# Kernel tuning notes

Measured on AMD Instinct MI355X. Metric: run time of the kernel, lower is better.

## Reference

```python
import jax, jax.numpy as jnp
import numpy as np

HIDDEN = 768
HEADS = 12
HEAD_DIM = HIDDEN // HEADS  # 64


def setup_inputs() -> dict:
    key = jax.random.key(0)
    ks = jax.random.split(key, 8)
    B, S = 2, 2048
    hidden_states = jax.random.normal(ks[0], (B, S, HIDDEN), dtype=jnp.float32)
    attention_mask = jnp.zeros((B, 1, 1, S), dtype=jnp.float32)
    scale = 1.0 / np.sqrt(HIDDEN)
    Wq = jax.random.normal(ks[1], (HIDDEN, HIDDEN), dtype=jnp.float32) * scale
    bq = jnp.zeros((HIDDEN,), dtype=jnp.float32)
    Wk = jax.random.normal(ks[2], (HIDDEN, HIDDEN), dtype=jnp.float32) * scale
    bk = jnp.zeros((HIDDEN,), dtype=jnp.float32)
    Wv = jax.random.normal(ks[3], (HIDDEN, HIDDEN), dtype=jnp.float32) * scale
    bv = jnp.zeros((HIDDEN,), dtype=jnp.float32)
    return {
        "hidden_states": hidden_states,
        "attention_mask": attention_mask,
        "Wq": Wq, "bq": bq, "Wk": Wk, "bk": bk, "Wv": Wv, "bv": bv,
    }


def _split_heads(x):
    # [B, S, hidden] -> [B, H, S, D]
    B, S, _ = x.shape
    return x.reshape(B, S, HEADS, HEAD_DIM).transpose(0, 2, 1, 3)


def reference(hidden_states, attention_mask, Wq, bq, Wk, bk, Wv, bv):
    q = _split_heads(hidden_states @ Wq + bq)  # [B,H,S,D]
    k = _split_heads(hidden_states @ Wk + bk)
    v = _split_heads(hidden_states @ Wv + bv)
    scores = jnp.einsum('bhqd,bhkd->bhqk', q, k) / np.sqrt(HEAD_DIM)
    scores = scores + attention_mask  # broadcast [B,1,1,S]
    probs = jax.nn.softmax(scores, axis=-1)
    ctx = jnp.einsum('bhqk,bhkd->bhqd', probs, v)  # [B,H,S,D]
    B, H, S, D = ctx.shape
    return ctx.transpose(0, 2, 1, 3).reshape(B, S, H * D)
```

## Files before the change

kernel.cpp:

```cpp
#include <hip/hip_runtime.h>

#define HID 768
#define NHEAD 12
#define HD 64
#define SEQ 2048
#define BATCH 2
#define PH (BATCH * NHEAD * SEQ * HD)
#define XEL (BATCH * SEQ * HID)
#define LOG2E 1.4426950408889634f
#define C1 (0.125f * LOG2E)

typedef __attribute__((ext_vector_type(8))) short bf16x8;
typedef __attribute__((ext_vector_type(4))) short bf16x4;
typedef __attribute__((ext_vector_type(4))) float f32x4;
typedef __attribute__((ext_vector_type(16))) float f32x16;

static __device__ __forceinline__ short f2b(float f) {
  unsigned int u = __builtin_bit_cast(unsigned int, f);
  unsigned int r = (u + 0x7fffu + ((u >> 16) & 1u)) >> 16;
  return (short)(unsigned short)r;
}

static __device__ __forceinline__ float fexp2(float x) {
  float r; asm("v_exp_f32 %0, %1" : "=v"(r) : "v"(x)); return r;
}

__global__ __launch_bounds__(256) void prep(
    const float* __restrict__ X,
    const float* __restrict__ Wq, const float* __restrict__ Wk,
    const float* __restrict__ Wv, const float* __restrict__ mask,
    short* __restrict__ Xb, short* __restrict__ Wt, float* __restrict__ mask2)
{
  __shared__ short T[64][65];
  const int t = threadIdx.x;
  const int blk = blockIdx.x;
  if (blk < 768) {
    const size_t base = (size_t)blk * 4096 + t * 16;
    f32x4 a0 = *(const f32x4*)(X + base);
    f32x4 a1 = *(const f32x4*)(X + base + 4);
    f32x4 a2 = *(const f32x4*)(X + base + 8);
    f32x4 a3 = *(const f32x4*)(X + base + 12);
    bf16x8 o0, o1;
#pragma unroll
    for (int i = 0; i < 4; ++i) {
      o0[i] = f2b(a0[i]); o0[4 + i] = f2b(a1[i]);
      o1[i] = f2b(a2[i]); o1[4 + i] = f2b(a3[i]);
    }
    *(bf16x8*)(Xb + base) = o0;
    *(bf16x8*)(Xb + base + 8) = o1;
  } else if (blk < 1200) {
    const int wb   = blk - 768;
    const int mat  = wb / 144;
    const int tile = wb - mat * 144;
    const int r0 = (tile / 12) * 64;
    const int c0 = (tile % 12) * 64;
    const float* __restrict__ W = (mat == 0) ? Wq : (mat == 1 ? Wk : Wv);
#pragma unroll
    for (int i = 0; i < 4; ++i) {
      const int r = (t >> 4) + 16 * i;
      const int c = (t & 15) * 4;
      f32x4 v = *(const f32x4*)(W + (size_t)(r0 + r) * HID + c0 + c);
      T[r][c + 0] = f2b(v[0]); T[r][c + 1] = f2b(v[1]);
      T[r][c + 2] = f2b(v[2]); T[r][c + 3] = f2b(v[3]);
    }
    __syncthreads();
    const int cr = t >> 2;
    const int ck = (t & 3) * 16;
    bf16x8 u0, u1;
#pragma unroll
    for (int j = 0; j < 8; ++j) { u0[j] = T[ck + j][cr]; u1[j] = T[ck + 8 + j][cr]; }
    short* orow = Wt + (size_t)(mat * HID + c0 + cr) * HID + r0 + ck;
    *(bf16x8*)orow = u0;
    *(bf16x8*)(orow + 8) = u1;
  } else {
#pragma unroll
    for (int i = 0; i < 4; ++i) {
      const int idx = (t * 4 + i * 1024);
      f32x4 v = *(const f32x4*)(mask + idx);
      v *= LOG2E;
      *(f32x4*)(mask2 + idx) = v;
    }
  }
}

__global__ __launch_bounds__(256, 3) void qkv_gemm(
    const short* __restrict__ Xb, const short* __restrict__ Wt,
    const float* __restrict__ bq, const float* __restrict__ bk,
    const float* __restrict__ bv,
    short* __restrict__ Qb, short* __restrict__ Kb, short* __restrict__ Vt)
{
  __shared__ __align__(16) short SM[128 * 132];
  short (*A_lds)[64] = (short(*)[64])SM;
  short (*B_lds)[64] = (short(*)[64])(SM + 128 * 64);
  short (*Tv)[132]   = (short(*)[132])SM;

  const int tid = threadIdx.x;
  const int w  = tid >> 6;
  const int l  = tid & 63;
  const int lr = l & 15;
  const int g  = l >> 4;
  const int wm = w >> 1;
  const int wn = w & 1;

  const int raw = blockIdx.x;
  const int swz = (raw & 7) * 72 + (raw >> 3);
  const int by  = swz / 18;
  const int bx  = swz - by * 18;
  const int mb0 = by * 128;
  const int nb0 = bx * 128;

  const int lrow8 = l >> 3;
  const int lslot = (l & 7) ^ lrow8;
  const short* __restrict__ pA = Xb + (size_t)(mb0 + w * 32 + lrow8) * HID + lslot * 8;
  const short* __restrict__ pB = Wt + (size_t)(nb0 + w * 32 + lrow8) * HID + lslot * 8;

  f32x4 acc[4][4];
#pragma unroll
  for (int mi = 0; mi < 4; ++mi)
#pragma unroll
    for (int ni = 0; ni < 4; ++ni) acc[mi][ni] = (f32x4){0.f, 0.f, 0.f, 0.f};

  const int rsw = (lr & 7) << 3;

  for (int ks = 0; ks < HID / 64; ++ks) {
    const int k0 = ks * 64;
    __syncthreads();
#pragma unroll
    for (int i = 0; i < 4; ++i) {
      __builtin_amdgcn_global_load_lds(
          (const void*)(pA + k0 + i * 8 * HID), (void*)&A_lds[w * 32 + i * 8][0], 16, 0, 0);
      __builtin_amdgcn_global_load_lds(
          (const void*)(pB + k0 + i * 8 * HID), (void*)&B_lds[w * 32 + i * 8][0], 16, 0, 0);
    }
    __syncthreads();

#pragma unroll
    for (int h = 0; h < 2; ++h) {
      bf16x8 a[4], b[4];
#pragma unroll
      for (int i = 0; i < 4; ++i) {
        const int coff = (((h << 2) | g) << 3) ^ rsw;
        a[i] = *(const bf16x8*)&A_lds[wm * 64 + 16 * i + lr][coff];
        b[i] = *(const bf16x8*)&B_lds[wn * 64 + 16 * i + lr][coff];
      }
#pragma unroll
      for (int mi = 0; mi < 4; ++mi)
#pragma unroll
        for (int ni = 0; ni < 4; ++ni)
          acc[mi][ni] = __builtin_amdgcn_mfma_f32_16x16x32_bf16(a[mi], b[ni], acc[mi][ni], 0, 0, 0);
    }
  }

  const int mat  = nb0 / HID;
  const int n0   = nb0 + wn * 64;
  const int m0   = mb0 + wm * 64;
  const int colb = n0 - mat * HID;

  if (mat < 2) {
    const float* __restrict__ bias = (mat == 0) ? bq : bk;
    short* __restrict__ Out        = (mat == 0) ? Qb : Kb;
#pragma unroll
    for (int ni = 0; ni < 4; ++ni) {
      const int col = colb + 16 * ni + lr;
      const int h = col >> 6, d = col & 63;
      const float bias_v = bias[col];
#pragma unroll
      for (int mi = 0; mi < 4; ++mi) {
        const int mbase = m0 + 16 * mi + 4 * g;
#pragma unroll
        for (int r = 0; r < 4; ++r) {
          const int m = mbase + r;
          const int bb = m >> 11;
          const int s  = m & (SEQ - 1);
          Out[((size_t)(bb * NHEAD + h) * SEQ + s) * HD + d] = f2b(acc[mi][ni][r] + bias_v);
        }
      }
    }
  } else {
    __syncthreads();
#pragma unroll
    for (int ni = 0; ni < 4; ++ni) {
      const int col = colb + 16 * ni + lr;
      const float bias_v = bv[col];
      const int rowl = wn * 64 + 16 * ni + lr;
#pragma unroll
      for (int mi = 0; mi < 4; ++mi) {
        bf16x4 pk;
#pragma unroll
        for (int r = 0; r < 4; ++r) pk[r] = f2b(acc[mi][ni][r] + bias_v);
        *(bf16x4*)&Tv[rowl][wm * 64 + 16 * mi + 4 * g] = pk;
      }
    }
    __syncthreads();
    const int row  = tid >> 1;
    const int half = tid & 1;
    const int col  = nb0 - 2 * HID + row;
    const int h = col >> 6, d = col & 63;
    const int bb = mb0 >> 11;
    const int s0 = (mb0 & (SEQ - 1)) + half * 64;
    short* op = Vt + ((size_t)(bb * NHEAD + h) * HD + d) * SEQ + s0;
#pragma unroll
    for (int j = 0; j < 8; ++j)
      *(bf16x8*)(op + 8 * j) = *(const bf16x8*)&Tv[row][half * 64 + 8 * j];
  }
}

__global__ __launch_bounds__(128, 4) void attn_fwd(
    const short* __restrict__ Qb, const short* __restrict__ Kb,
    const short* __restrict__ Vt, const float* __restrict__ mask2,
    float* __restrict__ out)
{
  __shared__ __align__(16) short K_lds[64][72];
  __shared__ __align__(16) short VT_lds[64][72];
  __shared__ __align__(16) short P_lds[2][32][72];

  const int tid = threadIdx.x;
  const int w   = tid >> 6;
  const int l   = tid & 63;
  const int r5  = l & 31;
  const int hi  = l >> 5;
  const int bh  = blockIdx.y;
  const int b   = bh / 12;
  const int hh  = bh - b * 12;
  const int q0  = blockIdx.x * 64 + w * 32;

  const short* __restrict__ Qh  = Qb + (size_t)bh * SEQ * HD;
  const short* __restrict__ Kh  = Kb + (size_t)bh * SEQ * HD;
  const short* __restrict__ Vth = Vt + (size_t)bh * HD * SEQ;
  const float* __restrict__ mb2 = mask2 + (size_t)b * SEQ;

  bf16x8 qf[4];
#pragma unroll
  for (int j = 0; j < 4; ++j)
    qf[j] = *(const bf16x8*)(Qh + (size_t)(q0 + r5) * HD + 16 * j + 8 * hi);

  f32x16 o0 = (f32x16){0.f};
  f32x16 o1 = (f32x16){0.f};
  float m2 = -INFINITY;
  float l_run = 0.f;

  const int sr = tid >> 1;
  const int sc = (tid & 1) * 32;
  const short* __restrict__ Kp = Kh + (size_t)sr * HD + sc;
  const short* __restrict__ Vp = Vth + (size_t)sr * SEQ + sc;

  bf16x8 kst[4], vst[4];
#pragma unroll
  for (int j = 0; j < 4; ++j) {
    kst[j] = *(const bf16x8*)(Kp + 8 * j);
    vst[j] = *(const bf16x8*)(Vp + 8 * j);
  }
#pragma unroll
  for (int j = 0; j < 4; ++j) {
    *(bf16x8*)&K_lds[sr][sc + 8 * j]  = kst[j];
    *(bf16x8*)&VT_lds[sr][sc + 8 * j] = vst[j];
  }

  for (int t = 0; t < SEQ / 64; ++t) {
    const int kv0 = t * 64;
    __syncthreads();

    const size_t kvn = (size_t)(((t + 1) & (SEQ / 64 - 1)) * 64);
#pragma unroll
    for (int j = 0; j < 4; ++j) {
      kst[j] = *(const bf16x8*)(Kp + kvn * HD + 8 * j);
      vst[j] = *(const bf16x8*)(Vp + kvn + 8 * j);
    }

    f32x16 st0 = (f32x16){0.f};
    f32x16 st1 = (f32x16){0.f};
    __builtin_amdgcn_s_setprio(1);
#pragma unroll
    for (int j = 0; j < 4; ++j) {
      bf16x8 ka0 = *(const bf16x8*)&K_lds[r5][16 * j + 8 * hi];
      bf16x8 ka1 = *(const bf16x8*)&K_lds[32 + r5][16 * j + 8 * hi];
      st0 = __builtin_amdgcn_mfma_f32_32x32x16_bf16(ka0, qf[j], st0, 0, 0, 0);
      st1 = __builtin_amdgcn_mfma_f32_32x32x16_bf16(ka1, qf[j], st1, 0, 0, 0);
    }
    __builtin_amdgcn_s_setprio(0);

    float p[2][16];
#pragma unroll
    for (int t2 = 0; t2 < 4; ++t2) {
      f32x4 mv0 = *(const f32x4*)&mb2[kv0 + 8 * t2 + 4 * hi];
      f32x4 mv1 = *(const f32x4*)&mb2[kv0 + 32 + 8 * t2 + 4 * hi];
#pragma unroll
      for (int e = 0; e < 4; ++e) {
        p[0][4 * t2 + e] = st0[4 * t2 + e] * C1 + mv0[e];
        p[1][4 * t2 + e] = st1[4 * t2 + e] * C1 + mv1[e];
      }
    }
    float mx[8];
#pragma unroll
    for (int i = 0; i < 8; ++i)
      mx[i] = fmaxf(fmaxf(p[0][2 * i], p[0][2 * i + 1]),
                    fmaxf(p[1][2 * i], p[1][2 * i + 1]));
    float tm = fmaxf(fmaxf(fmaxf(mx[0], mx[1]), fmaxf(mx[2], mx[3])),
                     fmaxf(fmaxf(mx[4], mx[5]), fmaxf(mx[6], mx[7])));
    tm = fmaxf(tm, __shfl_xor(tm, 32, 64));

    if (__any(tm > m2 + 8.f)) {
      const float mn = fmaxf(m2, tm);
      const float alpha = fexp2(m2 - mn);
      o0 *= alpha;
      o1 *= alpha;
      l_run *= alpha;
      m2 = mn;
    }

#pragma unroll
    for (int s2 = 0; s2 < 2; ++s2)
#pragma unroll
      for (int i = 0; i < 16; ++i) p[s2][i] = fexp2(p[s2][i] - m2);
    float sm[8];
#pragma unroll
    for (int i = 0; i < 8; ++i)
      sm[i] = (p[0][2 * i] + p[0][2 * i + 1]) + (p[1][2 * i] + p[1][2 * i + 1]);
    float ts = ((sm[0] + sm[1]) + (sm[2] + sm[3])) + ((sm[4] + sm[5]) + (sm[6] + sm[7]));
    ts += __shfl_xor(ts, 32, 64);
    l_run += ts;

#pragma unroll
    for (int s2 = 0; s2 < 2; ++s2)
#pragma unroll
      for (int t2 = 0; t2 < 4; ++t2) {
        unsigned int u0, u1;
        asm("v_cvt_pk_bf16_f32 %0, %1, %2"
            : "=v"(u0) : "v"(p[s2][4 * t2 + 0]), "v"(p[s2][4 * t2 + 1]));
        asm("v_cvt_pk_bf16_f32 %0, %1, %2"
            : "=v"(u1) : "v"(p[s2][4 * t2 + 2]), "v"(p[s2][4 * t2 + 3]));
        uint2 uv; uv.x = u0; uv.y = u1;
        *(uint2*)&P_lds[w][r5][32 * s2 + 8 * t2 + 4 * hi] = uv;
      }

    bf16x8 pf[4];
#pragma unroll
    for (int j = 0; j < 4; ++j)
      pf[j] = *(const bf16x8*)&P_lds[w][r5][16 * j + 8 * hi];

    __builtin_amdgcn_s_setprio(1);
#pragma unroll
    for (int j = 0; j < 4; ++j) {
      bf16x8 va0 = *(const bf16x8*)&VT_lds[r5][16 * j + 8 * hi];
      bf16x8 va1 = *(const bf16x8*)&VT_lds[32 + r5][16 * j + 8 * hi];
      o0 = __builtin_amdgcn_mfma_f32_32x32x16_bf16(va0, pf[j], o0, 0, 0, 0);
      o1 = __builtin_amdgcn_mfma_f32_32x32x16_bf16(va1, pf[j], o1, 0, 0, 0);
    }
    __builtin_amdgcn_s_setprio(0);

    __syncthreads();
#pragma unroll
    for (int j = 0; j < 4; ++j) {
      *(bf16x8*)&K_lds[sr][sc + 8 * j]  = kst[j];
      *(bf16x8*)&VT_lds[sr][sc + 8 * j] = vst[j];
    }
  }

  const float inv = 1.f / l_run;
  float* ob = out + (size_t)(b * SEQ + q0 + r5) * HID + hh * HD;
#pragma unroll
  for (int t2 = 0; t2 < 4; ++t2) {
    f32x4 v0, v1;
#pragma unroll
    for (int e = 0; e < 4; ++e) { v0[e] = o0[4 * t2 + e] * inv; v1[e] = o1[4 * t2 + e] * inv; }
    *(f32x4*)&ob[8 * t2 + 4 * hi]      = v0;
    *(f32x4*)&ob[32 + 8 * t2 + 4 * hi] = v1;
  }
}

extern "C" void kernel_launch(void* const* d_in, const int* in_sizes, int n_in,
                              void* d_out, int out_size, void* d_ws, size_t ws_size,
                              hipStream_t stream) {
  const float* X    = (const float*)d_in[0];
  const float* mask = (const float*)d_in[1];
  const float* Wq   = (const float*)d_in[2];
  const float* bq   = (const float*)d_in[3];
  const float* Wk   = (const float*)d_in[4];
  const float* bk   = (const float*)d_in[5];
  const float* Wv   = (const float*)d_in[6];
  const float* bv   = (const float*)d_in[7];
  float* out = (float*)d_out;

  short* Qb = (short*)d_ws;
  short* Kb = Qb + PH;
  short* Vt = Kb + PH;
  short* Xb = Vt + PH;
  short* Wt = Xb + XEL;
  float* mask2 = (float*)(Wt + (size_t)3 * HID * HID);

  prep<<<dim3(1201), 256, 0, stream>>>(X, Wq, Wk, Wv, mask, Xb, Wt, mask2);
  qkv_gemm<<<dim3(576), 256, 0, stream>>>(Xb, Wt, bq, bk, bv, Qb, Kb, Vt);
  attn_fwd<<<dim3(32, 24), 128, 0, stream>>>(Qb, Kb, Vt, mask2, out);
}
```

Baseline: 88.95 us.

## Split KV range across two wave pairs per block and merge softmax states

The attention kernel now launches 256 threads per block: two wave pairs each process half of the key/value sequence for the same 64 queries, then combine their partial outputs through LDS using max/sum rescaling. LDS tiles switch from padded rows to XOR-swizzled 64-wide rows to avoid bank conflicts. This doubles the waves available per query tile to hide latency. In exchange it adds an LDS reduction epilogue, more LDS per block and lower blocks-per-CU bounds.

```diff
diff --git a/kernel.cpp b/kernel.cpp
--- a/kernel.cpp
+++ b/kernel.cpp
@@ -205,24 +205,27 @@
   }
 }
 
-__global__ __launch_bounds__(128, 4) void attn_fwd(
+__global__ __launch_bounds__(256, 3) void attn_fwd(
     const short* __restrict__ Qb, const short* __restrict__ Kb,
     const short* __restrict__ Vt, const float* __restrict__ mask2,
     float* __restrict__ out)
 {
-  __shared__ __align__(16) short K_lds[64][72];
-  __shared__ __align__(16) short VT_lds[64][72];
-  __shared__ __align__(16) short P_lds[2][32][72];
-
-  const int tid = threadIdx.x;
-  const int w   = tid >> 6;
-  const int l   = tid & 63;
-  const int r5  = l & 31;
-  const int hi  = l >> 5;
-  const int bh  = blockIdx.y;
-  const int b   = bh / 12;
-  const int hh  = bh - b * 12;
-  const int q0  = blockIdx.x * 64 + w * 32;
+  __shared__ __align__(16) short KA[2][64][64];
+  __shared__ __align__(16) short VA[2][64][64];
+  __shared__ __align__(16) short PA[4][32][72];
+
+  const int tid  = threadIdx.x;
+  const int w    = tid >> 6;
+  const int pair = w >> 1;
+  const int pw   = w & 1;
+  const int l    = tid & 63;
+  const int r5   = l & 31;
+  const int hi   = l >> 5;
+  const int bh   = blockIdx.y;
+  const int b    = bh / 12;
+  const int hh   = bh - b * 12;
+  const int q0   = blockIdx.x * 64 + pw * 32;
+  const int kb   = pair * 1024;
 
   const short* __restrict__ Qh  = Qb + (size_t)bh * SEQ * HD;
   const short* __restrict__ Kh  = Kb + (size_t)bh * SEQ * HD;
@@ -236,13 +239,15 @@
 
   f32x16 o0 = (f32x16){0.f};
   f32x16 o1 = (f32x16){0.f};
-  float m2 = -INFINITY;
+  float mrun = -INFINITY;
   float l_run = 0.f;
 
-  const int sr = tid >> 1;
-  const int sc = (tid & 1) * 32;
-  const short* __restrict__ Kp = Kh + (size_t)sr * HD + sc;
-  const short* __restrict__ Vp = Vth + (size_t)sr * SEQ + sc;
+  const int ptid = tid & 127;
+  const int sr = ptid >> 1;
+  const int sb = (ptid & 1) * 4;
+  const short* __restrict__ Kp = Kh + (size_t)(kb + sr) * HD + sb * 8;
+  const short* __restrict__ Vp = Vth + (size_t)sr * SEQ + kb + sb * 8;
+  const int ssw = sr & 7;
 
   bf16x8 kst[4], vst[4];
 #pragma unroll
@@ -252,15 +257,17 @@
   }
 #pragma unroll
   for (int j = 0; j < 4; ++j) {
-    *(bf16x8*)&K_lds[sr][sc + 8 * j]  = kst[j];
-    *(bf16x8*)&VT_lds[sr][sc + 8 * j] = vst[j];
-  }
-
-  for (int t = 0; t < SEQ / 64; ++t) {
-    const int kv0 = t * 64;
-    __syncthreads();
-
-    const size_t kvn = (size_t)(((t + 1) & (SEQ / 64 - 1)) * 64);
+    *(bf16x8*)&KA[pair][sr][((sb + j) ^ ssw) * 8] = kst[j];
+    *(bf16x8*)&VA[pair][sr][((sb + j) ^ ssw) * 8] = vst[j];
+  }
+
+  const int rsw = r5 & 7;
+
+  for (int t = 0; t < 16; ++t) {
+    const int kv0 = kb + t * 64;
+    __syncthreads();
+
+    const size_t kvn = (size_t)(((t + 1) & 15) * 64);
 #pragma unroll
     for (int j = 0; j < 4; ++j) {
       kst[j] = *(const bf16x8*)(Kp + kvn * HD + 8 * j);
@@ -272,8 +279,9 @@
     __builtin_amdgcn_s_setprio(1);
 #pragma unroll
     for (int j = 0; j < 4; ++j) {
-      bf16x8 ka0 = *(const bf16x8*)&K_lds[r5][16 * j + 8 * hi];
-      bf16x8 ka1 = *(const bf16x8*)&K_lds[32 + r5][16 * j + 8 * hi];
+      const int co = ((2 * j + hi) ^ rsw) * 8;
+      bf16x8 ka0 = *(const bf16x8*)&KA[pair][r5][co];
+      bf16x8 ka1 = *(const bf16x8*)&KA[pair][32 + r5][co];
       st0 = __builtin_amdgcn_mfma_f32_32x32x16_bf16(ka0, qf[j], st0, 0, 0, 0);
       st1 = __builtin_amdgcn_mfma_f32_32x32x16_bf16(ka1, qf[j], st1, 0, 0, 0);
     }
@@ -299,19 +307,19 @@
                      fmaxf(fmaxf(mx[4], mx[5]), fmaxf(mx[6], mx[7])));
     tm = fmaxf(tm, __shfl_xor(tm, 32, 64));
 
-    if (__any(tm > m2 + 8.f)) {
-      const float mn = fmaxf(m2, tm);
-      const float alpha = fexp2(m2 - mn);
+    if (__any(tm > mrun + 8.f)) {
+      const float mn = fmaxf(mrun, tm);
+      const float alpha = fexp2(mrun - mn);
       o0 *= alpha;
       o1 *= alpha;
       l_run *= alpha;
-      m2 = mn;
+      mrun = mn;
     }
 
 #pragma unroll
     for (int s2 = 0; s2 < 2; ++s2)
 #pragma unroll
-      for (int i = 0; i < 16; ++i) p[s2][i] = fexp2(p[s2][i] - m2);
+      for (int i = 0; i < 16; ++i) p[s2][i] = fexp2(p[s2][i] - mrun);
     float sm[8];
 #pragma unroll
     for (int i = 0; i < 8; ++i)
@@ -330,19 +338,20 @@
         asm("v_cvt_pk_bf16_f32 %0, %1, %2"
             : "=v"(u1) : "v"(p[s2][4 * t2 + 2]), "v"(p[s2][4 * t2 + 3]));
         uint2 uv; uv.x = u0; uv.y = u1;
-        *(uint2*)&P_lds[w][r5][32 * s2 + 8 * t2 + 4 * hi] = uv;
+        *(uint2*)&PA[w][r5][32 * s2 + 8 * t2 + 4 * hi] = uv;
       }
 
     bf16x8 pf[4];
 #pragma unroll
     for (int j = 0; j < 4; ++j)
-      pf[j] = *(const bf16x8*)&P_lds[w][r5][16 * j + 8 * hi];
+      pf[j] = *(const bf16x8*)&PA[w][r5][16 * j + 8 * hi];
 
     __builtin_amdgcn_s_setprio(1);
 #pragma unroll
     for (int j = 0; j < 4; ++j) {
-      bf16x8 va0 = *(const bf16x8*)&VT_lds[r5][16 * j + 8 * hi];
-      bf16x8 va1 = *(const bf16x8*)&VT_lds[32 + r5][16 * j + 8 * hi];
+      const int co = ((2 * j + hi) ^ rsw) * 8;
+      bf16x8 va0 = *(const bf16x8*)&VA[pair][r5][co];
+      bf16x8 va1 = *(const bf16x8*)&VA[pair][32 + r5][co];
       o0 = __builtin_amdgcn_mfma_f32_32x32x16_bf16(va0, pf[j], o0, 0, 0, 0);
       o1 = __builtin_amdgcn_mfma_f32_32x32x16_bf16(va1, pf[j], o1, 0, 0, 0);
     }
@@ -351,20 +360,54 @@
     __syncthreads();
 #pragma unroll
     for (int j = 0; j < 4; ++j) {
-      *(bf16x8*)&K_lds[sr][sc + 8 * j]  = kst[j];
-      *(bf16x8*)&VT_lds[sr][sc + 8 * j] = vst[j];
-    }
-  }
-
-  const float inv = 1.f / l_run;
-  float* ob = out + (size_t)(b * SEQ + q0 + r5) * HID + hh * HD;
-#pragma unroll
-  for (int t2 = 0; t2 < 4; ++t2) {
-    f32x4 v0, v1;
-#pragma unroll
-    for (int e = 0; e < 4; ++e) { v0[e] = o0[4 * t2 + e] * inv; v1[e] = o1[4 * t2 + e] * inv; }
-    *(f32x4*)&ob[8 * t2 + 4 * hi]      = v0;
-    *(f32x4*)&ob[32 + 8 * t2 + 4 * hi] = v1;
+      *(bf16x8*)&KA[pair][sr][((sb + j) ^ ssw) * 8] = kst[j];
+      *(bf16x8*)&VA[pair][sr][((sb + j) ^ ssw) * 8] = vst[j];
+    }
+  }
+
+  __syncthreads();
+  float* Os = (float*)&KA[0][0][0];
+  float* ML = (float*)&PA[0][0][0];
+
+  if (w >= 2) {
+    const int wv = w - 2;
+    float* Or = Os + (size_t)(wv * 32 + r5) * 64;
+#pragma unroll
+    for (int t2 = 0; t2 < 4; ++t2) {
+      f32x4 v0, v1;
+#pragma unroll
+      for (int e = 0; e < 4; ++e) { v0[e] = o0[4 * t2 + e]; v1[e] = o1[4 * t2 + e]; }
+      *(f32x4*)&Or[8 * t2 + 4 * hi]      = v0;
+      *(f32x4*)&Or[32 + 8 * t2 + 4 * hi] = v1;
+    }
+    if (hi == 0) {
+      ML[wv * 64 + r5]      = mrun;
+      ML[wv * 64 + 32 + r5] = l_run;
+    }
+  }
+  __syncthreads();
+  if (w < 2) {
+    const float mo = ML[w * 64 + r5];
+    const float lo = ML[w * 64 + 32 + r5];
+    const float mm = fmaxf(mrun, mo);
+    const float a0 = fexp2(mrun - mm);
+    const float a1 = fexp2(mo - mm);
+    const float inv = 1.f / (a0 * l_run + a1 * lo);
+    const float* Or = Os + (size_t)(w * 32 + r5) * 64;
+    float* ob = out + (size_t)(b * SEQ + q0 + r5) * HID + hh * HD;
+#pragma unroll
+    for (int t2 = 0; t2 < 4; ++t2) {
+      f32x4 po = *(const f32x4*)&Or[8 * t2 + 4 * hi];
+      f32x4 p1 = *(const f32x4*)&Or[32 + 8 * t2 + 4 * hi];
+      f32x4 v0, v1;
+#pragma unroll
+      for (int e = 0; e < 4; ++e) {
+        v0[e] = (a0 * o0[4 * t2 + e] + a1 * po[e]) * inv;
+        v1[e] = (a0 * o1[4 * t2 + e] + a1 * p1[e]) * inv;
+      }
+      *(f32x4*)&ob[8 * t2 + 4 * hi]      = v0;
+      *(f32x4*)&ob[32 + 8 * t2 + 4 * hi] = v1;
+    }
   }
 }
 
@@ -390,5 +433,5 @@
 
   prep<<<dim3(1201), 256, 0, stream>>>(X, Wq, Wk, Wv, mask, Xb, Wt, mask2);
   qkv_gemm<<<dim3(576), 256, 0, stream>>>(Xb, Wt, bq, bk, bv, Qb, Kb, Vt);
-  attn_fwd<<<dim3(32, 24), 128, 0, stream>>>(Qb, Kb, Vt, mask2, out);
-}
+  attn_fwd<<<dim3(32, 24), 256, 0, stream>>>(Qb, Kb, Vt, mask2, out);
+}
```

Result: slower. 90.91 us (+2.2%).
